# Performance work log

Measured on AMD Instinct MI355X. Metric: run time of the kernel, lower is better.

Reference implementation:

```python
import jax, jax.numpy as jnp
import numpy as np

N_HEADS = 16
D_EMBD = 1024
B, T = 2, 2048


def setup_inputs() -> dict:
    key = jax.random.key(0)
    k1, k2, k3 = jax.random.split(key, 3)
    x = jax.random.normal(k1, (B, T, D_EMBD), dtype=jnp.float32)
    W1 = jax.random.normal(k2, (D_EMBD, 3 * D_EMBD), dtype=jnp.float32) / np.sqrt(D_EMBD)
    b1 = jnp.zeros((3 * D_EMBD,), dtype=jnp.float32)
    W2 = jax.random.normal(k3, (D_EMBD, D_EMBD), dtype=jnp.float32) / np.sqrt(D_EMBD)
    b2 = jnp.zeros((D_EMBD,), dtype=jnp.float32)
    return {"x": x, "W1": W1, "b1": b1, "W2": W2, "b2": b2}


def reference(x, W1, b1, W2, b2):
    bs, t, d = x.shape
    h = N_HEADS
    kqv = x @ W1 + b1  # [b, t, 3d]
    # note original split order: k, q, v
    k, q, v = jnp.split(kqv, 3, axis=-1)
    # [b, t, d] -> [b, h, t, dh]
    def to_heads(z):
        return z.reshape(bs, t, h, d // h).transpose(0, 2, 1, 3)
    k, q, v = to_heads(k), to_heads(q), to_heads(v)
    mask = jnp.tril(jnp.ones((t, t), dtype=bool))
    attn = jnp.where(mask, jnp.einsum('bhqd,bhkd->bhqk', q, k), 0.0)  # softmax-free retention
    out = jnp.einsum('bhqk,bhkd->bhqd', attn, v)
    out = out.transpose(0, 2, 1, 3).reshape(bs, t, d)  # [b, t, d]
    return out @ W2 + b2
```

## Files before the change

### kernel.cpp

```cpp
#include <hip/hip_runtime.h>
#include <hip/hip_bf16.h>

typedef __bf16 bf16x8 __attribute__((ext_vector_type(8)));
typedef float f32x4 __attribute__((ext_vector_type(4)));
typedef unsigned short ushort_t;
typedef unsigned short ushort8 __attribute__((ext_vector_type(8)));


__device__ inline void gload_lds16(const void* g, void* l) {
  __builtin_amdgcn_global_load_lds(
      (const __attribute__((address_space(1))) void*)g,
      (__attribute__((address_space(3))) void*)l, 16, 0, 0);
}

__device__ inline ushort_t f2bf(float f) {
  unsigned int u = __float_as_uint(f);
  unsigned int lsb = (u >> 16) & 1u;
  u += 0x7fffu + lsb;
  return (ushort_t)(u >> 16);
}


__global__ __launch_bounds__(256) void f32_to_bf16_vec(
    const float* __restrict__ in, ushort_t* __restrict__ out) {
  int i = (blockIdx.x * 256 + threadIdx.x) * 8;
  float4 a = *(const float4*)&in[i];
  float4 b = *(const float4*)&in[i + 4];
  ushort8 o;
  o[0] = f2bf(a.x); o[1] = f2bf(a.y); o[2] = f2bf(a.z); o[3] = f2bf(a.w);
  o[4] = f2bf(b.x); o[5] = f2bf(b.y); o[6] = f2bf(b.z); o[7] = f2bf(b.w);
  *(ushort8*)&out[i] = o;
}

__global__ __launch_bounds__(256) void transpose_f32_bf16(
    const float* __restrict__ in, ushort_t* __restrict__ out, int R, int C) {
  __shared__ float tile[32][33];
  const int tx = threadIdx.x & 31, ty = threadIdx.x >> 5;
  const int c0 = blockIdx.x * 32, r0 = blockIdx.y * 32;
#pragma unroll
  for (int i = 0; i < 32; i += 8)
    tile[ty + i][tx] = in[(size_t)(r0 + ty + i) * C + c0 + tx];
  __syncthreads();
#pragma unroll
  for (int i = 0; i < 32; i += 8)
    out[(size_t)(c0 + ty + i) * R + r0 + tx] = f2bf(tile[tx][ty + i]);
}

__global__ __launch_bounds__(256) void transpose_v(
    const ushort_t* __restrict__ kqv, ushort_t* __restrict__ vt) {
  __shared__ ushort_t tile[64 * 64];
  const int tt = blockIdx.x;
  const int bh = blockIdx.y;
  const int b = bh >> 4, h = bh & 15;
  const int tid = threadIdx.x;
#pragma unroll
  for (int p = 0; p < 2; p++) {
    const int tr = (tid >> 3) + p * 32;
    const int c8 = tid & 7;
    ushort8 v = *(const ushort8*)&kqv[(size_t)(b * 2048 + tt * 64 + tr) * 3072 +
                                      2048 + h * 64 + c8 * 8];
    *(ushort8*)&tile[tr * 64 + ((c8 ^ (tr & 7)) * 8)] = v;
  }
  __syncthreads();
  const int d = tid & 63;
#pragma unroll
  for (int p = 0; p < 2; p++) {
    const int t8 = (tid >> 6) + p * 4;
    ushort8 o;
#pragma unroll
    for (int j = 0; j < 8; j++) {
      const int t = t8 * 8 + j;
      o[j] = tile[t * 64 + (((d >> 3) ^ (t & 7)) * 8) + (d & 7)];
    }
    *(ushort8*)&vt[(size_t)(bh * 64 + d) * 2048 + tt * 64 + t8 * 8] = o;
  }
}


template <bool OUT_BF16>
__global__ __launch_bounds__(256) void gemm_bt(
    const ushort_t* __restrict__ A, const ushort_t* __restrict__ BT,
    const float* __restrict__ bias, void* __restrict__ Cout,
    int M, int N, int K) {
  __shared__ ushort_t lA[128 * 32];
  __shared__ ushort_t lB[128 * 32];
  const int tid = threadIdx.x;
  const int lane = tid & 63;
  const int wave = tid >> 6;
  const int wr = wave >> 1, wc = wave & 1;
  const int l16 = lane & 15, lhi = lane >> 4;
  const int bx = blockIdx.x, by = blockIdx.y;

  const ushort_t* gA = A + (size_t)(by * 128 + (tid >> 2)) * K + (tid & 3) * 8;
  const ushort_t* gB = BT + (size_t)(bx * 128 + (tid >> 2)) * K + (tid & 3) * 8;

  f32x4 acc[4][4] = {};

  for (int k0 = 0; k0 < K; k0 += 32) {
    gload_lds16(gA + k0, &lA[tid * 8]);
    gload_lds16(gA + k0 + (size_t)64 * K, &lA[tid * 8 + 2048]);
    gload_lds16(gB + k0, &lB[tid * 8]);
    gload_lds16(gB + k0 + (size_t)64 * K, &lB[tid * 8 + 2048]);
    __syncthreads();

    bf16x8 af[4], bfr[4];
#pragma unroll
    for (int m = 0; m < 4; m++)
      af[m] = *(const bf16x8*)&lA[(wr * 64 + m * 16 + l16) * 32 + lhi * 8];
#pragma unroll
    for (int n = 0; n < 4; n++)
      bfr[n] = *(const bf16x8*)&lB[(wc * 64 + n * 16 + l16) * 32 + lhi * 8];
#pragma unroll
    for (int m = 0; m < 4; m++)
#pragma unroll
      for (int n = 0; n < 4; n++)
        acc[m][n] = __builtin_amdgcn_mfma_f32_16x16x32_bf16(af[m], bfr[n],
                                                            acc[m][n], 0, 0, 0);
    __syncthreads();
  }

  const int r0 = by * 128 + wr * 64 + lhi * 4;
  const int c0 = bx * 128 + wc * 64 + l16;
#pragma unroll
  for (int m = 0; m < 4; m++)
#pragma unroll
    for (int n = 0; n < 4; n++) {
      const int col = c0 + n * 16;
      const float bv = bias[col];
#pragma unroll
      for (int j = 0; j < 4; j++) {
        const int row = r0 + m * 16 + j;
        const float v = acc[m][n][j] + bv;
        if (OUT_BF16)
          ((ushort_t*)Cout)[(size_t)row * N + col] = f2bf(v);
        else
          ((float*)Cout)[(size_t)row * N + col] = v;
      }
    }
}


__global__ __launch_bounds__(512) void attn_kernel(
    const ushort_t* __restrict__ kqv, const ushort_t* __restrict__ vt,
    ushort_t* __restrict__ ao) {
  __shared__ ushort_t lK[3][64 * 64];
  __shared__ ushort_t lVT[3][64 * 64];
  __shared__ ushort_t lS[8][16 * 64];
  const int tid = threadIdx.x, lane = tid & 63, wave = tid >> 6;
  const int l16 = lane & 15, lhi = lane >> 4;
  const int L = blockIdx.x;
  const int W = (L & 7) * 64 + (L >> 3);
  const int qi = 15 - (W & 15);
  const int bh = W >> 4;
  const int b = bh >> 4, h = bh & 15;
  const int q0 = qi * 128;
  const ushort_t* base = kqv + (size_t)b * 2048 * 3072;
  const ushort_t* vbase = vt + (size_t)bh * 64 * 2048;

  const int srow = tid >> 3;
  const int scb_src = ((tid & 7) * 16) ^ ((srow & 7) << 4);
  const size_t kg = (size_t)srow * 3072 + h * 64 + (scb_src >> 1);
  const size_t vg = (size_t)srow * 2048 + (scb_src >> 1);

  const int wq0 = q0 + wave * 16;
  bf16x8 qf[2];
#pragma unroll
  for (int ks = 0; ks < 2; ks++)
    qf[ks] = *(const bf16x8*)&base[(size_t)(wq0 + l16) * 3072 + 1024 + h * 64 +
                                   ks * 32 + lhi * 8];

  f32x4 oacc[4] = {};
  const int nkt = q0 / 64 + 2;

  gload_lds16(&base[kg], &lK[0][tid * 8]);
  gload_lds16(&vbase[vg], &lVT[0][tid * 8]);
  gload_lds16(&base[(size_t)64 * 3072 + kg], &lK[1][tid * 8]);
  gload_lds16(&vbase[64 + vg], &lVT[1][tid * 8]);

  int cur = 0;
  for (int kt = 0; kt < nkt; ++kt) {
    if (kt + 1 < nkt) asm volatile("s_waitcnt vmcnt(2)" ::: "memory");
    else              asm volatile("s_waitcnt vmcnt(0)" ::: "memory");
    __builtin_amdgcn_s_barrier();
    asm volatile("" ::: "memory");

    if (kt + 2 < nkt) {
      const int pf = (cur + 2 >= 3) ? cur - 1 : cur + 2;
      gload_lds16(&base[(size_t)(kt + 2) * 64 * 3072 + kg], &lK[pf][tid * 8]);
      gload_lds16(&vbase[(size_t)(kt + 2) * 64 + vg], &lVT[pf][tid * 8]);
    }

    if (kt * 64 <= wq0 + 15) {
      f32x4 sacc[4] = {};
#pragma unroll
      for (int n = 0; n < 4; n++) {
        const int kr = n * 16 + l16;
        const int sw = (kr & 7) << 3;
        bf16x8 kf0 = *(const bf16x8*)&lK[cur][kr * 64 + ((lhi * 8) ^ sw)];
        bf16x8 kf1 = *(const bf16x8*)&lK[cur][kr * 64 + ((32 + lhi * 8) ^ sw)];
        sacc[n] = __builtin_amdgcn_mfma_f32_16x16x32_bf16(qf[0], kf0, sacc[n], 0, 0, 0);
        sacc[n] = __builtin_amdgcn_mfma_f32_16x16x32_bf16(qf[1], kf1, sacc[n], 0, 0, 0);
      }

      const bool need_mask = (kt * 64 + 63) > wq0;
#pragma unroll
      for (int n = 0; n < 4; n++)
#pragma unroll
        for (int j = 0; j < 4; j++) {
          float s = sacc[n][j];
          const int r = lhi * 4 + j;
          if (need_mask && (kt * 64 + n * 16 + l16) > (wq0 + r)) s = 0.f;
          __bf16 hv = (__bf16)s;
          lS[wave][r * 64 + ((n * 16 + l16) ^ ((r & 7) << 3))] =
              __builtin_bit_cast(ushort_t, hv);
        }

#pragma unroll
      for (int ks = 0; ks < 2; ks++) {
        bf16x8 sf = *(const bf16x8*)&lS[wave][l16 * 64 +
                                              ((ks * 32 + lhi * 8) ^ ((l16 & 7) << 3))];
#pragma unroll
        for (int n = 0; n < 4; n++) {
          const int dr = n * 16 + l16;
          bf16x8 vf = *(const bf16x8*)&lVT[cur][dr * 64 +
                                                ((ks * 32 + lhi * 8) ^ ((dr & 7) << 3))];
          oacc[n] = __builtin_amdgcn_mfma_f32_16x16x32_bf16(sf, vf, oacc[n], 0, 0, 0);
        }
      }
    }

    cur = (cur + 1 >= 3) ? 0 : cur + 1;
  }

#pragma unroll
  for (int n = 0; n < 4; n++)
#pragma unroll
    for (int j = 0; j < 4; j++) {
      const int row = wq0 + lhi * 4 + j;
      const int col = h * 64 + n * 16 + l16;
      ao[(size_t)(b * 2048 + row) * 1024 + col] = f2bf(oacc[n][j]);
    }
}


extern "C" void kernel_launch(void* const* d_in, const int* in_sizes, int n_in,
                              void* d_out, int out_size, void* d_ws, size_t ws_size,
                              hipStream_t stream) {
  const float* x  = (const float*)d_in[0];
  const float* W1 = (const float*)d_in[1];
  const float* b1 = (const float*)d_in[2];
  const float* W2 = (const float*)d_in[3];
  const float* b2 = (const float*)d_in[4];
  float* out = (float*)d_out;

  char* ws = (char*)d_ws;
  ushort_t* xb  = (ushort_t*)(ws);
  ushort_t* w1t = (ushort_t*)(ws + 8388608);
  ushort_t* w2t = (ushort_t*)(ws + 14680064);
  ushort_t* kqv = (ushort_t*)(ws + 16777216);
  ushort_t* ao  = (ushort_t*)(ws + 41943040);
  ushort_t* vtb = (ushort_t*)(ws);

  f32_to_bf16_vec<<<2048, 256, 0, stream>>>(x, xb);
  transpose_f32_bf16<<<dim3(96, 32), 256, 0, stream>>>(W1, w1t, 1024, 3072);
  transpose_f32_bf16<<<dim3(32, 32), 256, 0, stream>>>(W2, w2t, 1024, 1024);
  gemm_bt<true ><<<dim3(24, 32), 256, 0, stream>>>(xb, w1t, b1, kqv, 4096, 3072, 1024);
  transpose_v<<<dim3(32, 32), 256, 0, stream>>>(kqv, vtb);
  attn_kernel<<<dim3(512), 512, 0, stream>>>(kqv, vtb, ao);
  gemm_bt<false><<<dim3(8, 32), 256, 0, stream>>>(ao, w2t, b2, out, 4096, 1024, 1024);
}
```

Measured before the change: 209.3 us.

## Switch attention to 32x32 MFMA with register-resident score transpose

The attention kernel now has 4 waves, each owning 32 query rows instead of 16, and computes S^T with 32x32x16 bf16 MFMA. Scores are converted with packed bf16 conversion and rearranged through permlane32 swaps so they can feed the PV MFMA directly from registers, which removes the per-wave LDS staging buffer for scores. Each thread now issues two global-to-LDS loads per tile. The intent is to cut LDS round-trips and raise MFMA efficiency. In exchange there are fewer waves per block, more accumulator registers per thread, and more lanes doing masked work on diagonal tiles.

```diff
diff --git a/kernel.cpp b/kernel.cpp
--- a/kernel.cpp
+++ b/kernel.cpp
@@ -3,8 +3,10 @@
 
 typedef __bf16 bf16x8 __attribute__((ext_vector_type(8)));
 typedef float f32x4 __attribute__((ext_vector_type(4)));
+typedef float f32x16 __attribute__((ext_vector_type(16)));
 typedef unsigned short ushort_t;
 typedef unsigned short ushort8 __attribute__((ext_vector_type(8)));
+typedef unsigned int uint4v __attribute__((ext_vector_type(4)));
 
 
 __device__ inline void gload_lds16(const void* g, void* l) {
@@ -140,14 +142,13 @@
 }
 
 
-__global__ __launch_bounds__(512) void attn_kernel(
+__global__ __launch_bounds__(256) void attn_kernel(
     const ushort_t* __restrict__ kqv, const ushort_t* __restrict__ vt,
     ushort_t* __restrict__ ao) {
   __shared__ ushort_t lK[3][64 * 64];
   __shared__ ushort_t lVT[3][64 * 64];
-  __shared__ ushort_t lS[8][16 * 64];
   const int tid = threadIdx.x, lane = tid & 63, wave = tid >> 6;
-  const int l16 = lane & 15, lhi = lane >> 4;
+  const int q_rel = lane & 31, hi = lane >> 5;
   const int L = blockIdx.x;
   const int W = (L & 7) * 64 + (L >> 3);
   const int qi = 15 - (W & 15);
@@ -157,74 +158,105 @@
   const ushort_t* base = kqv + (size_t)b * 2048 * 3072;
   const ushort_t* vbase = vt + (size_t)bh * 64 * 2048;
 
-  const int srow = tid >> 3;
-  const int scb_src = ((tid & 7) * 16) ^ ((srow & 7) << 4);
-  const size_t kg = (size_t)srow * 3072 + h * 64 + (scb_src >> 1);
-  const size_t vg = (size_t)srow * 2048 + (scb_src >> 1);
-
-  const int wq0 = q0 + wave * 16;
-  bf16x8 qf[2];
-#pragma unroll
-  for (int ks = 0; ks < 2; ks++)
-    qf[ks] = *(const bf16x8*)&base[(size_t)(wq0 + l16) * 3072 + 1024 + h * 64 +
-                                   ks * 32 + lhi * 8];
-
-  f32x4 oacc[4] = {};
-  const int nkt = q0 / 64 + 2;
-
-  gload_lds16(&base[kg], &lK[0][tid * 8]);
-  gload_lds16(&vbase[vg], &lVT[0][tid * 8]);
-  gload_lds16(&base[(size_t)64 * 3072 + kg], &lK[1][tid * 8]);
-  gload_lds16(&vbase[64 + vg], &lVT[1][tid * 8]);
+  size_t kg[2], vg[2];
+  int ld[2];
+#pragma unroll
+  for (int p = 0; p < 2; p++) {
+    const int slot = tid + p * 256;
+    const int srow = slot >> 3;
+    const int scb = (((slot & 7) * 16) ^ ((srow & 7) << 4)) >> 1;
+    kg[p] = (size_t)srow * 3072 + h * 64 + scb;
+    vg[p] = (size_t)srow * 2048 + scb;
+    ld[p] = slot * 8;
+  }
+
+  const int wq0 = q0 + wave * 32;
+  bf16x8 qf[4];
+#pragma unroll
+  for (int ds = 0; ds < 4; ds++)
+    qf[ds] = *(const bf16x8*)&base[(size_t)(wq0 + q_rel) * 3072 + 1024 + h * 64 +
+                                   ds * 16 + hi * 8];
+
+  f32x16 oacc[2] = {};
+  const int nkt = qi * 2 + 2;
+
+#pragma unroll
+  for (int p = 0; p < 2; p++) {
+    gload_lds16(&base[kg[p]], &lK[0][ld[p]]);
+    gload_lds16(&vbase[vg[p]], &lVT[0][ld[p]]);
+  }
+#pragma unroll
+  for (int p = 0; p < 2; p++) {
+    gload_lds16(&base[(size_t)64 * 3072 + kg[p]], &lK[1][ld[p]]);
+    gload_lds16(&vbase[64 + vg[p]], &lVT[1][ld[p]]);
+  }
 
   int cur = 0;
   for (int kt = 0; kt < nkt; ++kt) {
-    if (kt + 1 < nkt) asm volatile("s_waitcnt vmcnt(2)" ::: "memory");
+    if (kt + 1 < nkt) asm volatile("s_waitcnt vmcnt(4)" ::: "memory");
     else              asm volatile("s_waitcnt vmcnt(0)" ::: "memory");
     __builtin_amdgcn_s_barrier();
     asm volatile("" ::: "memory");
 
     if (kt + 2 < nkt) {
       const int pf = (cur + 2 >= 3) ? cur - 1 : cur + 2;
-      gload_lds16(&base[(size_t)(kt + 2) * 64 * 3072 + kg], &lK[pf][tid * 8]);
-      gload_lds16(&vbase[(size_t)(kt + 2) * 64 + vg], &lVT[pf][tid * 8]);
-    }
-
-    if (kt * 64 <= wq0 + 15) {
-      f32x4 sacc[4] = {};
-#pragma unroll
-      for (int n = 0; n < 4; n++) {
-        const int kr = n * 16 + l16;
-        const int sw = (kr & 7) << 3;
-        bf16x8 kf0 = *(const bf16x8*)&lK[cur][kr * 64 + ((lhi * 8) ^ sw)];
-        bf16x8 kf1 = *(const bf16x8*)&lK[cur][kr * 64 + ((32 + lhi * 8) ^ sw)];
-        sacc[n] = __builtin_amdgcn_mfma_f32_16x16x32_bf16(qf[0], kf0, sacc[n], 0, 0, 0);
-        sacc[n] = __builtin_amdgcn_mfma_f32_16x16x32_bf16(qf[1], kf1, sacc[n], 0, 0, 0);
+#pragma unroll
+      for (int p = 0; p < 2; p++) {
+        gload_lds16(&base[(size_t)(kt + 2) * 64 * 3072 + kg[p]], &lK[pf][ld[p]]);
+        gload_lds16(&vbase[(size_t)(kt + 2) * 64 + vg[p]], &lVT[pf][ld[p]]);
       }
-
+    }
+
+    if (kt * 64 <= wq0 + 31) {
       const bool need_mask = (kt * 64 + 63) > wq0;
 #pragma unroll
-      for (int n = 0; n < 4; n++)
-#pragma unroll
-        for (int j = 0; j < 4; j++) {
-          float s = sacc[n][j];
-          const int r = lhi * 4 + j;
-          if (need_mask && (kt * 64 + n * 16 + l16) > (wq0 + r)) s = 0.f;
-          __bf16 hv = (__bf16)s;
-          lS[wave][r * 64 + ((n * 16 + l16) ^ ((r & 7) << 3))] =
-              __builtin_bit_cast(ushort_t, hv);
+      for (int kb = 0; kb < 2; kb++) {
+        f32x16 st = {};
+        const int krow = kb * 32 + q_rel;
+        const int ksw = krow & 7;
+#pragma unroll
+        for (int ds = 0; ds < 4; ds++) {
+          bf16x8 kf = *(const bf16x8*)&lK[cur][krow * 64 + (((ds * 2 + hi) ^ ksw) * 8)];
+          st = __builtin_amdgcn_mfma_f32_32x32x16_bf16(kf, qf[ds], st, 0, 0, 0);
         }
-
-#pragma unroll
-      for (int ks = 0; ks < 2; ks++) {
-        bf16x8 sf = *(const bf16x8*)&lS[wave][l16 * 64 +
-                                              ((ks * 32 + lhi * 8) ^ ((l16 & 7) << 3))];
-#pragma unroll
-        for (int n = 0; n < 4; n++) {
-          const int dr = n * 16 + l16;
-          bf16x8 vf = *(const bf16x8*)&lVT[cur][dr * 64 +
-                                                ((ks * 32 + lhi * 8) ^ ((dr & 7) << 3))];
-          oacc[n] = __builtin_amdgcn_mfma_f32_16x16x32_bf16(sf, vf, oacc[n], 0, 0, 0);
+        if (need_mask) {
+#pragma unroll
+          for (int r = 0; r < 16; r++) {
+            const int kgl = kt * 64 + kb * 32 + (r & 3) + 8 * (r >> 2) + 4 * hi;
+            if (kgl > wq0 + q_rel) st[r] = 0.f;
+          }
+        }
+        unsigned int w0, w1, w2, w3, w4, w5, w6, w7;
+        {
+          float e0 = st[0], e1 = st[1], e2 = st[2], e3 = st[3];
+          float e4 = st[4], e5 = st[5], e6 = st[6], e7 = st[7];
+          float e8 = st[8], e9 = st[9], e10 = st[10], e11 = st[11];
+          float e12 = st[12], e13 = st[13], e14 = st[14], e15 = st[15];
+          asm("v_cvt_pk_bf16_f32 %0, %1, %2" : "=v"(w0) : "v"(e0), "v"(e1));
+          asm("v_cvt_pk_bf16_f32 %0, %1, %2" : "=v"(w1) : "v"(e2), "v"(e3));
+          asm("v_cvt_pk_bf16_f32 %0, %1, %2" : "=v"(w2) : "v"(e4), "v"(e5));
+          asm("v_cvt_pk_bf16_f32 %0, %1, %2" : "=v"(w3) : "v"(e6), "v"(e7));
+          asm("v_cvt_pk_bf16_f32 %0, %1, %2" : "=v"(w4) : "v"(e8), "v"(e9));
+          asm("v_cvt_pk_bf16_f32 %0, %1, %2" : "=v"(w5) : "v"(e10), "v"(e11));
+          asm("v_cvt_pk_bf16_f32 %0, %1, %2" : "=v"(w6) : "v"(e12), "v"(e13));
+          asm("v_cvt_pk_bf16_f32 %0, %1, %2" : "=v"(w7) : "v"(e14), "v"(e15));
+        }
+        asm("v_permlane32_swap_b32 %0, %1" : "+v"(w0), "+v"(w2));
+        asm("v_permlane32_swap_b32 %0, %1" : "+v"(w1), "+v"(w3));
+        asm("v_permlane32_swap_b32 %0, %1" : "+v"(w4), "+v"(w6));
+        asm("v_permlane32_swap_b32 %0, %1" : "+v"(w5), "+v"(w7));
+        uint4v u0 = {w0, w1, w2, w3};
+        uint4v u1 = {w4, w5, w6, w7};
+        bf16x8 pa0 = __builtin_bit_cast(bf16x8, u0);
+        bf16x8 pa1 = __builtin_bit_cast(bf16x8, u1);
+#pragma unroll
+        for (int dt = 0; dt < 2; dt++) {
+          const int vrow = dt * 32 + q_rel;
+          const int vsw = vrow & 7;
+          bf16x8 vf0 = *(const bf16x8*)&lVT[cur][vrow * 64 + (((kb * 4 + hi) ^ vsw) * 8)];
+          bf16x8 vf1 = *(const bf16x8*)&lVT[cur][vrow * 64 + (((kb * 4 + 2 + hi) ^ vsw) * 8)];
+          oacc[dt] = __builtin_amdgcn_mfma_f32_32x32x16_bf16(pa0, vf0, oacc[dt], 0, 0, 0);
+          oacc[dt] = __builtin_amdgcn_mfma_f32_32x32x16_bf16(pa1, vf1, oacc[dt], 0, 0, 0);
         }
       }
     }
@@ -233,12 +265,13 @@
   }
 
 #pragma unroll
-  for (int n = 0; n < 4; n++)
-#pragma unroll
-    for (int j = 0; j < 4; j++) {
-      const int row = wq0 + lhi * 4 + j;
-      const int col = h * 64 + n * 16 + l16;
-      ao[(size_t)(b * 2048 + row) * 1024 + col] = f2bf(oacc[n][j]);
+  for (int dt = 0; dt < 2; dt++)
+#pragma unroll
+    for (int r = 0; r < 16; r++) {
+      const int q = (r & 3) + 8 * (r >> 2) + 4 * hi;
+      const int row = wq0 + q;
+      const int col = h * 64 + dt * 32 + q_rel;
+      ao[(size_t)(b * 2048 + row) * 1024 + col] = f2bf(oacc[dt][r]);
     }
 }
 
@@ -266,6 +299,6 @@
   transpose_f32_bf16<<<dim3(32, 32), 256, 0, stream>>>(W2, w2t, 1024, 1024);
   gemm_bt<true ><<<dim3(24, 32), 256, 0, stream>>>(xb, w1t, b1, kqv, 4096, 3072, 1024);
   transpose_v<<<dim3(32, 32), 256, 0, stream>>>(kqv, vtb);
-  attn_kernel<<<dim3(512), 512, 0, stream>>>(kqv, vtb, ao);
+  attn_kernel<<<dim3(512), 256, 0, stream>>>(kqv, vtb, ao);
   gemm_bt<false><<<dim3(8, 32), 256, 0, stream>>>(ao, w2t, b2, out, 4096, 1024, 1024);
 }
```

Result: no change. 209.7 us (+0.2%).
